# Kernel tuning notes

Hardware: AMD Instinct MI355X
Metric: run time of the kernel (lower is better)

## Reference

```python
import jax, jax.numpy as jnp
import numpy as np

NUM_STAB = 0.001  # numerical_stabilizer from relu_kernel_transformation


def relu_kernel(data, proj):
    """ReLU random-feature kernel: data [B,L,H,D], proj [M,D] -> [B,L,H,M]."""
    ratio = 1.0 / jnp.sqrt(jnp.asarray(proj.shape[0], jnp.float32))
    data_dash = ratio * jnp.einsum('blhd,md->blhm', data, proj)
    return jax.nn.relu(data_dash) + NUM_STAB


def setup_inputs() -> dict:
    key = jax.random.key(0)
    k1, k2, k3, k4 = jax.random.split(key, 4)
    B, L, H, D, M = 2, 4096, 8, 64, 256
    return {
        'query': jax.random.normal(k1, (B, L, H, D), jnp.float32),
        'key_t': jax.random.normal(k2, (B, L, H, D), jnp.float32),
        'value': jax.random.normal(k3, (B, L, H, D), jnp.float32),
        'projection_matrix': jax.random.normal(k4, (M, D), jnp.float32),
    }


def reference(query, key_t, value, projection_matrix):
    # Kernel feature maps [B,L,H,M]
    qp = relu_kernel(query, projection_matrix)
    kp = relu_kernel(key_t, projection_matrix)
    # Causal path operates in [L,B,H,*] layout
    qs = jnp.transpose(qp, (1, 0, 2, 3))     # [L,B,H,M]
    ks = jnp.transpose(kp, (1, 0, 2, 3))     # [L,B,H,M]
    vs = jnp.transpose(value, (1, 0, 2, 3))  # [L,B,H,D]

    B, H, M = qs.shape[1], qs.shape[2], qs.shape[3]
    D = vs.shape[3]
    init = (jnp.zeros((B, H, M, D), qs.dtype),  # running sum of k outer v
            jnp.zeros((B, H, M), qs.dtype))     # running sum of k

    def step(carry, inp):
        kv_sum, k_sum = carry
        q, k, v = inp  # [B,H,M], [B,H,M], [B,H,D]
        kv_sum = kv_sum + k[..., None] * v[..., None, :]
        k_sum = k_sum + k
        num = jnp.einsum('bhmd,bhm->bhd', kv_sum, q)  # causal numerator step
        den = jnp.einsum('bhm,bhm->bh', q, k_sum)     # causal denominator step
        return (kv_sum, k_sum), (num, den)

    _, (num, den) = jax.lax.scan(step, init, (qs, ks, vs))  # num [L,B,H,D], den [L,B,H]
    den = den[..., None]
    den = jnp.where(den <= 0.0, jnp.ones_like(den), den)
    out = num / den                      # [L,B,H,D]
    return jnp.transpose(out, (1, 0, 2, 3))  # [B,L,H,D]
```

## Files before the change

### kernel.cpp

```cpp
#include <hip/hip_runtime.h>
#include <hip/hip_bf16.h>


#define B_   2
#define L_   4096
#define H_   8
#define D_   64
#define M_   256
#define T_   128
#define C_   (L_ / T_)
#define NBH  (B_ * H_)
#define RATIO 0.0625f
#define STAB  0.001f
#define SVT  136
#define SQS  72

typedef __attribute__((ext_vector_type(8))) short short8;
typedef __attribute__((ext_vector_type(4))) float floatx4;

#define MFMA16(a, b, c) __builtin_amdgcn_mfma_f32_16x16x32_bf16(a, b, c, 0, 0, 0)

__device__ inline unsigned short f2bf(float x) {
    union { float f; unsigned u; } v; v.f = x;
    unsigned r = v.u + 0x7FFF + ((v.u >> 16) & 1);
    return (unsigned short)(r >> 16);
}
__device__ inline unsigned pack2bf(float a, float b) {
    __hip_bfloat162 h = __float22bfloat162_rn(make_float2(a, b));
    unsigned u; __builtin_memcpy(&u, &h, 4);
    return u;
}
__device__ inline short8 ldg8_bfs(const float* p) {
    float4 a = *(const float4*)p;
    float4 b = *(const float4*)(p + 4);
    short8 r;
    r[0] = (short)f2bf(a.x * RATIO); r[1] = (short)f2bf(a.y * RATIO);
    r[2] = (short)f2bf(a.z * RATIO); r[3] = (short)f2bf(a.w * RATIO);
    r[4] = (short)f2bf(b.x * RATIO); r[5] = (short)f2bf(b.y * RATIO);
    r[6] = (short)f2bf(b.z * RATIO); r[7] = (short)f2bf(b.w * RATIO);
    return r;
}
__device__ inline short8 ldg8_bf(const float* p) {
    float4 a = *(const float4*)p;
    float4 b = *(const float4*)(p + 4);
    short8 r;
    r[0] = (short)f2bf(a.x); r[1] = (short)f2bf(a.y);
    r[2] = (short)f2bf(a.z); r[3] = (short)f2bf(a.w);
    r[4] = (short)f2bf(b.x); r[5] = (short)f2bf(b.y);
    r[6] = (short)f2bf(b.z); r[7] = (short)f2bf(b.w);
    return r;
}

__global__ __launch_bounds__(512, 2)
void chunk_kernel(const float* __restrict__ key, const float* __restrict__ val,
                  const float* __restrict__ proj,
                  unsigned short* __restrict__ VTg, unsigned short* __restrict__ Pbf,
                  float* __restrict__ Ppart, float* __restrict__ Zpart) {
    const int c = blockIdx.x, bh = blockIdx.y;
    const int b = bh / H_, h = bh % H_;
    const int tid = threadIdx.x;
    const int w = tid >> 6, lane = tid & 63;
    const int l15 = lane & 15, quad = lane >> 4;

    __shared__ __align__(16) unsigned short SH[128 * SVT];
    __shared__ __align__(16) unsigned short KbfL[T_ * D_];
    unsigned short* VT  = SH;
    unsigned short* KpT = SH;

    const size_t rowstr = H_ * D_;
    const size_t base = ((size_t)b * L_ + (size_t)c * T_) * rowstr + (size_t)h * D_;

    for (int i = tid; i < T_ * 8; i += 512) {
        int t = i >> 3, d8 = (i & 7) * 8;
        short8 kv = ldg8_bfs(key + base + (size_t)t * rowstr + d8);
        int rt = t >> 4, l = t & 15, kk = d8 >> 5, q = (d8 & 31) >> 3;
        *(short8*)&KbfL[((rt * 2 + kk) * 64 + q * 16 + l) << 3] = kv;
    }
    for (int i = tid; i < T_ * 16; i += 512) {
        int t = i >> 4, d4 = (i & 15) * 4;
        float4 vv = *(const float4*)(val + base + (size_t)t * rowstr + d4);
        VT[(d4 + 0) * SVT + t] = f2bf(vv.x);
        VT[(d4 + 1) * SVT + t] = f2bf(vv.y);
        VT[(d4 + 2) * SVT + t] = f2bf(vv.z);
        VT[(d4 + 3) * SVT + t] = f2bf(vv.w);
    }
    __syncthreads();
    unsigned short* vout = VTg + ((size_t)bh * C_ + c) * (D_ * T_);
    for (int i = tid; i < D_ * 16; i += 512) {
        int d = i >> 4, tt = (i & 15) * 8;
        *(uint4*)(vout + d * T_ + tt) = *(const uint4*)&VT[d * SVT + tt];
    }
    const int dt_w = w >> 1;
    const int mt0 = (w & 1) * 4;
    short8 vf[4];
#pragma unroll
    for (int k4 = 0; k4 < 4; ++k4)
        vf[k4] = *(const short8*)&VT[(dt_w * 16 + l15) * SVT + k4 * 32 + quad * 8];
    if (c == 0 && tid < 256) {
        int i = bh * 256 + tid;
        float4 pv = *(const float4*)(proj + (size_t)i * 4);
        uint2 o; o.x = pack2bf(pv.x, pv.y); o.y = pack2bf(pv.z, pv.w);
        *(uint2*)(Pbf + (size_t)i * 4) = o;
    }
    __syncthreads();

    float* Pp = Ppart + ((size_t)bh * C_ + c) * (D_ * M_);

    for (int half = 0; half < 2; ++half) {
        const int mrow = half * 128 + w * 16 + l15;
        short8 pf0 = ldg8_bf(proj + (size_t)mrow * D_ + quad * 8);
        short8 pf1 = ldg8_bf(proj + (size_t)mrow * D_ + 32 + quad * 8);
        if (half) __syncthreads();
        float zp = 0.f;
#pragma unroll
        for (int rt = 0; rt < 8; ++rt) {
            short8 kf0 = *(const short8*)&KbfL[((rt * 2 + 0) * 64 + lane) << 3];
            short8 kf1 = *(const short8*)&KbfL[((rt * 2 + 1) * 64 + lane) << 3];
            floatx4 a = {0.f, 0.f, 0.f, 0.f};
            a = MFMA16(kf0, pf0, a);
            a = MFMA16(kf1, pf1, a);
            float k0 = fmaxf(a[0], 0.f) + STAB;
            float k1 = fmaxf(a[1], 0.f) + STAB;
            float k2 = fmaxf(a[2], 0.f) + STAB;
            float k3 = fmaxf(a[3], 0.f) + STAB;
            zp += (k0 + k1) + (k2 + k3);
            uint2 pk; pk.x = pack2bf(k0, k1); pk.y = pack2bf(k2, k3);
            *(uint2*)&KpT[(w * 16 + l15) * SVT + rt * 16 + quad * 4] = pk;
        }
        zp += __shfl_xor(zp, 16, 64);
        zp += __shfl_xor(zp, 32, 64);
        if (quad == 0)
            Zpart[((size_t)bh * C_ + c) * M_ + mrow] = zp;
        __syncthreads();

#pragma unroll
        for (int mt = 0; mt < 4; ++mt) {
            floatx4 acc = {0.f, 0.f, 0.f, 0.f};
#pragma unroll
            for (int k4 = 0; k4 < 4; ++k4) {
                short8 kb = *(const short8*)&KpT[((mt0 + mt) * 16 + l15) * SVT
                                                 + k4 * 32 + quad * 8];
                acc = MFMA16(vf[k4], kb, acc);
            }
            const int mcol = half * 128 + (mt0 + mt) * 16 + l15;
#pragma unroll
            for (int r = 0; r < 4; ++r)
                Pp[(size_t)(dt_w * 16 + quad * 4 + r) * M_ + mcol] = acc[r];
        }
    }
}

__global__ __launch_bounds__(256, 4)
void prefix_kernel(const float* __restrict__ Ppart, const float* __restrict__ Zpart,
                   unsigned short* __restrict__ S, float* __restrict__ Z) {
    const int g = blockIdx.x, bh = blockIdx.y;
    const int tid = threadIdx.x;
    if (g < 32) {
        const size_t dm = ((size_t)g * 256 + tid) * 2;
        const float* Pp = Ppart + (size_t)bh * C_ * (D_ * M_) + dm;
        unsigned short* Sp = S + (size_t)bh * C_ * (D_ * M_) + dm;
        float accx = 0.f, accy = 0.f;
#pragma unroll 8
        for (int c = 0; c < C_; ++c) {
            float2 p = *(const float2*)(Pp + (size_t)c * (D_ * M_));
            *(unsigned*)(Sp + (size_t)c * (D_ * M_)) = pack2bf(accx, accy);
            accx += p.x; accy += p.y;
        }
    } else {
        const float* Zp = Zpart + (size_t)bh * C_ * M_ + tid;
        float* Zo = Z + (size_t)bh * C_ * M_ + tid;
        float acc = 0.f;
#pragma unroll 8
        for (int c = 0; c < C_; ++c) {
            float z = Zp[(size_t)c * M_];
            Zo[(size_t)c * M_] = acc;
            acc += z;
        }
    }
}

__global__ __launch_bounds__(512, 2)
void phase3_kernel(const float* __restrict__ q, const float* __restrict__ key,
                   const unsigned short* __restrict__ VTg,
                   const unsigned short* __restrict__ Pbf,
                   const unsigned short* __restrict__ S, const float* __restrict__ Z,
                   float* __restrict__ out) {
    const int c = blockIdx.x, bh = blockIdx.y;
    const int b = bh / H_, h = bh % H_;
    const int tid = threadIdx.x;
    const int w = tid >> 6, lane = tid & 63;
    const int l15 = lane & 15, quad = lane >> 4;

    __shared__ __align__(16) unsigned short KpL[T_ * SVT];
    __shared__ __align__(16) unsigned short QpS[8 * 16 * SQS];

    const size_t rowstr = H_ * D_;
    const size_t base = ((size_t)b * L_ + (size_t)c * T_) * rowstr + (size_t)h * D_;
    const unsigned short* Sp = S + (size_t)(bh * C_ + c) * (M_ * D_);
    const float* Zp = Z + (size_t)(bh * C_ + c) * M_;
    const unsigned short* Vc = VTg + ((size_t)bh * C_ + c) * (D_ * T_);

    short8 qf[2], kf[2];
#pragma unroll
    for (int kk = 0; kk < 2; ++kk) {
        size_t ro = base + (size_t)(16 * w + l15) * rowstr + kk * 32 + quad * 8;
        qf[kk] = ldg8_bfs(q + ro);
        kf[kk] = ldg8_bfs(key + ro);
    }

    unsigned short* myQp = QpS + w * 16 * SQS;
    floatx4 num[4];
    floatx4 Aacc[8];
#pragma unroll
    for (int dt = 0; dt < 4; ++dt) { floatx4 z4 = {0.f,0.f,0.f,0.f}; num[dt] = z4; }
#pragma unroll
    for (int ct = 0; ct < 8; ++ct) { floatx4 z4 = {0.f,0.f,0.f,0.f}; Aacc[ct] = z4; }
    float dz[4] = {0.f, 0.f, 0.f, 0.f};

    for (int hh = 0; hh < 2; ++hh) {
        short8 qa[4];
#pragma unroll
        for (int fgl = 0; fgl < 2; ++fgl) {
            const int fg = 2 * hh + fgl;
#pragma unroll
            for (int ct = 0; ct < 4; ++ct) {
                const unsigned short* pp = Pbf + (size_t)(fg * 64 + ct * 16 + l15) * D_;
                short8 pf0 = *(const short8*)(pp + quad * 8);
                short8 pf1 = *(const short8*)(pp + 32 + quad * 8);
                floatx4 aq = {0.f, 0.f, 0.f, 0.f};
                aq = MFMA16(qf[0], pf0, aq);
                aq = MFMA16(qf[1], pf1, aq);
                floatx4 ak = {0.f, 0.f, 0.f, 0.f};
                ak = MFMA16(kf[0], pf0, ak);
                ak = MFMA16(kf[1], pf1, ak);
                const int mloc = fgl * 64 + ct * 16 + l15;
                float zv = Zp[hh * 128 + mloc];
#pragma unroll
                for (int r = 0; r < 4; ++r) {
                    float qpv = fmaxf(aq[r], 0.f) + STAB;
                    float kpv = fmaxf(ak[r], 0.f) + STAB;
                    myQp[(quad * 4 + r) * SQS + ct * 16 + l15] = f2bf(qpv);
                    KpL[(size_t)(16 * w + quad * 4 + r) * SVT + mloc] = f2bf(kpv);
                    dz[r] = fmaf(qpv, zv, dz[r]);
                }
            }
#pragma unroll
            for (int kk = 0; kk < 2; ++kk)
                qa[fgl * 2 + kk] = *(const short8*)&myQp[l15 * SQS + kk * 32 + quad * 8];
        }
#pragma unroll
        for (int dt = 0; dt < 4; ++dt)
#pragma unroll
            for (int kc = 0; kc < 4; ++kc) {
                short8 sb = *(const short8*)(Sp + (size_t)(dt * 16 + l15) * M_
                                             + hh * 128 + kc * 32 + quad * 8);
                num[dt] = MFMA16(qa[kc], sb, num[dt]);
            }
        __syncthreads();
#pragma unroll
        for (int ct = 0; ct < 8; ++ct) {
            if (ct <= w) {
#pragma unroll
                for (int kc = 0; kc < 4; ++kc) {
                    short8 kb = *(const short8*)&KpL[(size_t)(ct * 16 + l15) * SVT
                                                     + kc * 32 + quad * 8];
                    Aacc[ct] = MFMA16(qa[kc], kb, Aacc[ct]);
                }
            }
        }
        __syncthreads();
    }
#pragma unroll
    for (int r = 0; r < 4; ++r) {
        dz[r] += __shfl_xor(dz[r], 1, 64);
        dz[r] += __shfl_xor(dz[r], 2, 64);
        dz[r] += __shfl_xor(dz[r], 4, 64);
        dz[r] += __shfl_xor(dz[r], 8, 64);
    }

    unsigned short* AmL = KpL;
    float da[4] = {0.f, 0.f, 0.f, 0.f};
#pragma unroll
    for (int ct = 0; ct < 8; ++ct)
#pragma unroll
        for (int r = 0; r < 4; ++r) {
            float av = Aacc[ct][r];
            if (ct > w || (ct == w && l15 > quad * 4 + r)) av = 0.f;
            AmL[(size_t)(16 * w + quad * 4 + r) * SVT + ct * 16 + l15] = f2bf(av);
            da[r] += av;
        }
#pragma unroll
    for (int r = 0; r < 4; ++r) {
        da[r] += __shfl_xor(da[r], 1, 64);
        da[r] += __shfl_xor(da[r], 2, 64);
        da[r] += __shfl_xor(da[r], 4, 64);
        da[r] += __shfl_xor(da[r], 8, 64);
    }

    for (int k4 = 0; k4 <= (w >> 1); ++k4) {
        short8 am = *(const short8*)&AmL[(size_t)(16 * w + l15) * SVT
                                         + k4 * 32 + quad * 8];
#pragma unroll
        for (int dt = 0; dt < 4; ++dt) {
            short8 vb = *(const short8*)(Vc + (size_t)(dt * 16 + l15) * T_
                                         + k4 * 32 + quad * 8);
            num[dt] = MFMA16(am, vb, num[dt]);
        }
    }

#pragma unroll
    for (int r = 0; r < 4; ++r) {
        float den = da[r] + dz[r];
        if (den <= 0.f) den = 1.f;
        float inv = 1.f / den;
        int t = 16 * w + quad * 4 + r;
#pragma unroll
        for (int dt = 0; dt < 4; ++dt)
            out[base + (size_t)t * rowstr + dt * 16 + l15] = num[dt][r] * inv;
    }
}

extern "C" void kernel_launch(void* const* d_in, const int* in_sizes, int n_in,
                              void* d_out, int out_size, void* d_ws, size_t ws_size,
                              hipStream_t stream) {
    const float* q    = (const float*)d_in[0];
    const float* k    = (const float*)d_in[1];
    const float* v    = (const float*)d_in[2];
    const float* proj = (const float*)d_in[3];
    float* out = (float*)d_out;

    const size_t nS = (size_t)NBH * C_ * D_ * M_;
    const size_t nZ = (size_t)NBH * C_ * M_;
    const size_t nV = (size_t)NBH * C_ * D_ * T_;
    unsigned short* S     = (unsigned short*)d_ws;
    float*          Z     = (float*)(S + nS);
    unsigned short* VTg   = (unsigned short*)(Z + nZ);
    unsigned short* Pbf   = VTg + nV;
    float*          Ppart = (float*)(Pbf + (size_t)M_ * D_);
    float*          Zpart = Ppart + nS;

    chunk_kernel<<<dim3(C_, NBH), dim3(512), 0, stream>>>(k, v, proj, VTg, Pbf, Ppart, Zpart);
    prefix_kernel<<<dim3(33, NBH), dim3(256), 0, stream>>>(Ppart, Zpart, S, Z);
    phase3_kernel<<<dim3(C_, NBH), dim3(512), 0, stream>>>(q, k, VTg, Pbf, S, Z, out);
}
```

Baseline: 157.1 us.

## Fuse three phases into one cooperative persistent kernel with grid syncs

Merges the chunk, prefix-scan and output kernels into one cooperative kernel of 256 blocks, each handling two (chunk, bh) tiles, with grid-wide syncs between phases. The bf16 key tile is kept in shared memory across phases so the output phase does not reload and reconvert keys from global memory. This removes two kernel launches and their gaps. In exchange it runs at one block per CU, uses more LDS, and pays for two grid barriers.

```diff
diff --git a/kernel.cpp b/kernel.cpp
--- a/kernel.cpp
+++ b/kernel.cpp
@@ -1,5 +1,8 @@
 #include <hip/hip_runtime.h>
 #include <hip/hip_bf16.h>
+#include <hip/hip_cooperative_groups.h>
+
+namespace cg = cooperative_groups;
 
 
 #define B_   2
@@ -51,272 +54,279 @@
     return r;
 }
 
-__global__ __launch_bounds__(512, 2)
-void chunk_kernel(const float* __restrict__ key, const float* __restrict__ val,
-                  const float* __restrict__ proj,
+__global__ __launch_bounds__(512, 1)
+void fused_kernel(const float* __restrict__ q, const float* __restrict__ key,
+                  const float* __restrict__ val, const float* __restrict__ proj,
                   unsigned short* __restrict__ VTg, unsigned short* __restrict__ Pbf,
-                  float* __restrict__ Ppart, float* __restrict__ Zpart) {
-    const int c = blockIdx.x, bh = blockIdx.y;
-    const int b = bh / H_, h = bh % H_;
+                  float* __restrict__ Ppart, float* __restrict__ Zpart,
+                  unsigned short* __restrict__ S, float* __restrict__ Z,
+                  float* __restrict__ out) {
+    cg::grid_group grid = cg::this_grid();
+    const int fid = blockIdx.x;
     const int tid = threadIdx.x;
     const int w = tid >> 6, lane = tid & 63;
     const int l15 = lane & 15, quad = lane >> 4;
 
+    __shared__ __align__(16) unsigned short Kbf2[2][T_ * D_];
     __shared__ __align__(16) unsigned short SH[128 * SVT];
-    __shared__ __align__(16) unsigned short KbfL[T_ * D_];
-    unsigned short* VT  = SH;
-    unsigned short* KpT = SH;
+    __shared__ __align__(16) unsigned short QpS[8 * 16 * SQS];
 
     const size_t rowstr = H_ * D_;
-    const size_t base = ((size_t)b * L_ + (size_t)c * T_) * rowstr + (size_t)h * D_;
-
-    for (int i = tid; i < T_ * 8; i += 512) {
-        int t = i >> 3, d8 = (i & 7) * 8;
-        short8 kv = ldg8_bfs(key + base + (size_t)t * rowstr + d8);
-        int rt = t >> 4, l = t & 15, kk = d8 >> 5, q = (d8 & 31) >> 3;
-        *(short8*)&KbfL[((rt * 2 + kk) * 64 + q * 16 + l) << 3] = kv;
+
+    for (int pi = 0; pi < 2; ++pi) {
+        if (pi) __syncthreads();
+        const int p = fid + pi * 256;
+        const int c = p & 31, bh = p >> 5;
+        const int b = bh / H_, h = bh % H_;
+        const size_t base = ((size_t)b * L_ + (size_t)c * T_) * rowstr + (size_t)h * D_;
+        unsigned short* VT  = SH;
+        unsigned short* KpT = SH;
+        unsigned short* KbfL = Kbf2[pi];
+
+        for (int i = tid; i < T_ * 8; i += 512) {
+            int t = i >> 3, d8 = (i & 7) * 8;
+            short8 kv = ldg8_bfs(key + base + (size_t)t * rowstr + d8);
+            int rt = t >> 4, l = t & 15, kk = d8 >> 5, qq = (d8 & 31) >> 3;
+            *(short8*)&KbfL[((rt * 2 + kk) * 64 + qq * 16 + l) << 3] = kv;
+        }
+        for (int i = tid; i < T_ * 16; i += 512) {
+            int t = i >> 4, d4 = (i & 15) * 4;
+            float4 vv = *(const float4*)(val + base + (size_t)t * rowstr + d4);
+            VT[(d4 + 0) * SVT + t] = f2bf(vv.x);
+            VT[(d4 + 1) * SVT + t] = f2bf(vv.y);
+            VT[(d4 + 2) * SVT + t] = f2bf(vv.z);
+            VT[(d4 + 3) * SVT + t] = f2bf(vv.w);
+        }
+        __syncthreads();
+        unsigned short* vout = VTg + ((size_t)bh * C_ + c) * (D_ * T_);
+        for (int i = tid; i < D_ * 16; i += 512) {
+            int d = i >> 4, tt = (i & 15) * 8;
+            *(uint4*)(vout + d * T_ + tt) = *(const uint4*)&VT[d * SVT + tt];
+        }
+        const int dt_w = w >> 1;
+        const int mt0 = (w & 1) * 4;
+        short8 vf[4];
+#pragma unroll
+        for (int k4 = 0; k4 < 4; ++k4)
+            vf[k4] = *(const short8*)&VT[(dt_w * 16 + l15) * SVT + k4 * 32 + quad * 8];
+        if (c == 0 && tid < 256) {
+            int i = bh * 256 + tid;
+            float4 pv = *(const float4*)(proj + (size_t)i * 4);
+            uint2 o; o.x = pack2bf(pv.x, pv.y); o.y = pack2bf(pv.z, pv.w);
+            *(uint2*)(Pbf + (size_t)i * 4) = o;
+        }
+        __syncthreads();
+
+        float* Pp = Ppart + ((size_t)bh * C_ + c) * (D_ * M_);
+
+        for (int half = 0; half < 2; ++half) {
+            const int mrow = half * 128 + w * 16 + l15;
+            short8 pf0 = ldg8_bf(proj + (size_t)mrow * D_ + quad * 8);
+            short8 pf1 = ldg8_bf(proj + (size_t)mrow * D_ + 32 + quad * 8);
+            if (half) __syncthreads();
+            float zp = 0.f;
+#pragma unroll
+            for (int rt = 0; rt < 8; ++rt) {
+                short8 kf0 = *(const short8*)&KbfL[((rt * 2 + 0) * 64 + lane) << 3];
+                short8 kf1 = *(const short8*)&KbfL[((rt * 2 + 1) * 64 + lane) << 3];
+                floatx4 a = {0.f, 0.f, 0.f, 0.f};
+                a = MFMA16(kf0, pf0, a);
+                a = MFMA16(kf1, pf1, a);
+                float k0 = fmaxf(a[0], 0.f) + STAB;
+                float k1 = fmaxf(a[1], 0.f) + STAB;
+                float k2 = fmaxf(a[2], 0.f) + STAB;
+                float k3 = fmaxf(a[3], 0.f) + STAB;
+                zp += (k0 + k1) + (k2 + k3);
+                uint2 pk; pk.x = pack2bf(k0, k1); pk.y = pack2bf(k2, k3);
+                *(uint2*)&KpT[(w * 16 + l15) * SVT + rt * 16 + quad * 4] = pk;
+            }
+            zp += __shfl_xor(zp, 16, 64);
+            zp += __shfl_xor(zp, 32, 64);
+            if (quad == 0)
+                Zpart[((size_t)bh * C_ + c) * M_ + mrow] = zp;
+            __syncthreads();
+
+#pragma unroll
+            for (int mt = 0; mt < 4; ++mt) {
+                floatx4 acc = {0.f, 0.f, 0.f, 0.f};
+#pragma unroll
+                for (int k4 = 0; k4 < 4; ++k4) {
+                    short8 kb = *(const short8*)&KpT[((mt0 + mt) * 16 + l15) * SVT
+                                                     + k4 * 32 + quad * 8];
+                    acc = MFMA16(vf[k4], kb, acc);
+                }
+                const int mcol = half * 128 + (mt0 + mt) * 16 + l15;
+#pragma unroll
+                for (int r = 0; r < 4; ++r)
+                    Pp[(size_t)(dt_w * 16 + quad * 4 + r) * M_ + mcol] = acc[r];
+            }
+        }
     }
-    for (int i = tid; i < T_ * 16; i += 512) {
-        int t = i >> 4, d4 = (i & 15) * 4;
-        float4 vv = *(const float4*)(val + base + (size_t)t * rowstr + d4);
-        VT[(d4 + 0) * SVT + t] = f2bf(vv.x);
-        VT[(d4 + 1) * SVT + t] = f2bf(vv.y);
-        VT[(d4 + 2) * SVT + t] = f2bf(vv.z);
-        VT[(d4 + 3) * SVT + t] = f2bf(vv.w);
+    __threadfence();
+    grid.sync();
+
+    {
+        const size_t DM = (size_t)D_ * M_;
+        for (int it = 0; it < 2; ++it) {
+            size_t col = ((size_t)(it * 256 + fid)) * 512 + tid;
+            int bh = (int)(col >> 14);
+            size_t dm = col & (DM - 1);
+            const float* Pp = Ppart + (size_t)bh * C_ * DM + dm;
+            unsigned short* Sp = S + (size_t)bh * C_ * DM + dm;
+            float acc = 0.f;
+#pragma unroll 8
+            for (int cc = 0; cc < C_; ++cc) {
+                float pv = Pp[(size_t)cc * DM];
+                Sp[(size_t)cc * DM] = f2bf(acc);
+                acc += pv;
+            }
+        }
+        if (fid < 8) {
+            int zcol = fid * 512 + tid;
+            int bh = zcol >> 8, m = zcol & 255;
+            const float* Zp = Zpart + (size_t)bh * C_ * M_ + m;
+            float* Zo = Z + (size_t)bh * C_ * M_ + m;
+            float acc = 0.f;
+#pragma unroll 8
+            for (int cc = 0; cc < C_; ++cc) {
+                float zv = Zp[(size_t)cc * M_];
+                Zo[(size_t)cc * M_] = acc;
+                acc += zv;
+            }
+        }
     }
-    __syncthreads();
-    unsigned short* vout = VTg + ((size_t)bh * C_ + c) * (D_ * T_);
-    for (int i = tid; i < D_ * 16; i += 512) {
-        int d = i >> 4, tt = (i & 15) * 8;
-        *(uint4*)(vout + d * T_ + tt) = *(const uint4*)&VT[d * SVT + tt];
-    }
-    const int dt_w = w >> 1;
-    const int mt0 = (w & 1) * 4;
-    short8 vf[4];
-#pragma unroll
-    for (int k4 = 0; k4 < 4; ++k4)
-        vf[k4] = *(const short8*)&VT[(dt_w * 16 + l15) * SVT + k4 * 32 + quad * 8];
-    if (c == 0 && tid < 256) {
-        int i = bh * 256 + tid;
-        float4 pv = *(const float4*)(proj + (size_t)i * 4);
-        uint2 o; o.x = pack2bf(pv.x, pv.y); o.y = pack2bf(pv.z, pv.w);
-        *(uint2*)(Pbf + (size_t)i * 4) = o;
-    }
-    __syncthreads();
-
-    float* Pp = Ppart + ((size_t)bh * C_ + c) * (D_ * M_);
-
-    for (int half = 0; half < 2; ++half) {
-        const int mrow = half * 128 + w * 16 + l15;
-        short8 pf0 = ldg8_bf(proj + (size_t)mrow * D_ + quad * 8);
-        short8 pf1 = ldg8_bf(proj + (size_t)mrow * D_ + 32 + quad * 8);
-        if (half) __syncthreads();
-        float zp = 0.f;
-#pragma unroll
-        for (int rt = 0; rt < 8; ++rt) {
-            short8 kf0 = *(const short8*)&KbfL[((rt * 2 + 0) * 64 + lane) << 3];
-            short8 kf1 = *(const short8*)&KbfL[((rt * 2 + 1) * 64 + lane) << 3];
-            floatx4 a = {0.f, 0.f, 0.f, 0.f};
-            a = MFMA16(kf0, pf0, a);
-            a = MFMA16(kf1, pf1, a);
-            float k0 = fmaxf(a[0], 0.f) + STAB;
-            float k1 = fmaxf(a[1], 0.f) + STAB;
-            float k2 = fmaxf(a[2], 0.f) + STAB;
-            float k3 = fmaxf(a[3], 0.f) + STAB;
-            zp += (k0 + k1) + (k2 + k3);
-            uint2 pk; pk.x = pack2bf(k0, k1); pk.y = pack2bf(k2, k3);
-            *(uint2*)&KpT[(w * 16 + l15) * SVT + rt * 16 + quad * 4] = pk;
-        }
-        zp += __shfl_xor(zp, 16, 64);
-        zp += __shfl_xor(zp, 32, 64);
-        if (quad == 0)
-            Zpart[((size_t)bh * C_ + c) * M_ + mrow] = zp;
-        __syncthreads();
-
-#pragma unroll
-        for (int mt = 0; mt < 4; ++mt) {
-            floatx4 acc = {0.f, 0.f, 0.f, 0.f};
-#pragma unroll
-            for (int k4 = 0; k4 < 4; ++k4) {
-                short8 kb = *(const short8*)&KpT[((mt0 + mt) * 16 + l15) * SVT
-                                                 + k4 * 32 + quad * 8];
-                acc = MFMA16(vf[k4], kb, acc);
-            }
-            const int mcol = half * 128 + (mt0 + mt) * 16 + l15;
-#pragma unroll
-            for (int r = 0; r < 4; ++r)
-                Pp[(size_t)(dt_w * 16 + quad * 4 + r) * M_ + mcol] = acc[r];
-        }
-    }
-}
-
-__global__ __launch_bounds__(256, 4)
-void prefix_kernel(const float* __restrict__ Ppart, const float* __restrict__ Zpart,
-                   unsigned short* __restrict__ S, float* __restrict__ Z) {
-    const int g = blockIdx.x, bh = blockIdx.y;
-    const int tid = threadIdx.x;
-    if (g < 32) {
-        const size_t dm = ((size_t)g * 256 + tid) * 2;
-        const float* Pp = Ppart + (size_t)bh * C_ * (D_ * M_) + dm;
-        unsigned short* Sp = S + (size_t)bh * C_ * (D_ * M_) + dm;
-        float accx = 0.f, accy = 0.f;
-#pragma unroll 8
-        for (int c = 0; c < C_; ++c) {
-            float2 p = *(const float2*)(Pp + (size_t)c * (D_ * M_));
-            *(unsigned*)(Sp + (size_t)c * (D_ * M_)) = pack2bf(accx, accy);
-            accx += p.x; accy += p.y;
-        }
-    } else {
-        const float* Zp = Zpart + (size_t)bh * C_ * M_ + tid;
-        float* Zo = Z + (size_t)bh * C_ * M_ + tid;
-        float acc = 0.f;
-#pragma unroll 8
-        for (int c = 0; c < C_; ++c) {
-            float z = Zp[(size_t)c * M_];
-            Zo[(size_t)c * M_] = acc;
-            acc += z;
-        }
-    }
-}
-
-__global__ __launch_bounds__(512, 2)
-void phase3_kernel(const float* __restrict__ q, const float* __restrict__ key,
-                   const unsigned short* __restrict__ VTg,
-                   const unsigned short* __restrict__ Pbf,
-                   const unsigned short* __restrict__ S, const float* __restrict__ Z,
-                   float* __restrict__ out) {
-    const int c = blockIdx.x, bh = blockIdx.y;
-    const int b = bh / H_, h = bh % H_;
-    const int tid = threadIdx.x;
-    const int w = tid >> 6, lane = tid & 63;
-    const int l15 = lane & 15, quad = lane >> 4;
-
-    __shared__ __align__(16) unsigned short KpL[T_ * SVT];
-    __shared__ __align__(16) unsigned short QpS[8 * 16 * SQS];
-
-    const size_t rowstr = H_ * D_;
-    const size_t base = ((size_t)b * L_ + (size_t)c * T_) * rowstr + (size_t)h * D_;
-    const unsigned short* Sp = S + (size_t)(bh * C_ + c) * (M_ * D_);
-    const float* Zp = Z + (size_t)(bh * C_ + c) * M_;
-    const unsigned short* Vc = VTg + ((size_t)bh * C_ + c) * (D_ * T_);
-
-    short8 qf[2], kf[2];
-#pragma unroll
-    for (int kk = 0; kk < 2; ++kk) {
-        size_t ro = base + (size_t)(16 * w + l15) * rowstr + kk * 32 + quad * 8;
-        qf[kk] = ldg8_bfs(q + ro);
-        kf[kk] = ldg8_bfs(key + ro);
-    }
-
-    unsigned short* myQp = QpS + w * 16 * SQS;
-    floatx4 num[4];
-    floatx4 Aacc[8];
-#pragma unroll
-    for (int dt = 0; dt < 4; ++dt) { floatx4 z4 = {0.f,0.f,0.f,0.f}; num[dt] = z4; }
-#pragma unroll
-    for (int ct = 0; ct < 8; ++ct) { floatx4 z4 = {0.f,0.f,0.f,0.f}; Aacc[ct] = z4; }
-    float dz[4] = {0.f, 0.f, 0.f, 0.f};
-
-    for (int hh = 0; hh < 2; ++hh) {
-        short8 qa[4];
-#pragma unroll
-        for (int fgl = 0; fgl < 2; ++fgl) {
-            const int fg = 2 * hh + fgl;
-#pragma unroll
-            for (int ct = 0; ct < 4; ++ct) {
-                const unsigned short* pp = Pbf + (size_t)(fg * 64 + ct * 16 + l15) * D_;
-                short8 pf0 = *(const short8*)(pp + quad * 8);
-                short8 pf1 = *(const short8*)(pp + 32 + quad * 8);
-                floatx4 aq = {0.f, 0.f, 0.f, 0.f};
-                aq = MFMA16(qf[0], pf0, aq);
-                aq = MFMA16(qf[1], pf1, aq);
-                floatx4 ak = {0.f, 0.f, 0.f, 0.f};
-                ak = MFMA16(kf[0], pf0, ak);
-                ak = MFMA16(kf[1], pf1, ak);
-                const int mloc = fgl * 64 + ct * 16 + l15;
-                float zv = Zp[hh * 128 + mloc];
-#pragma unroll
-                for (int r = 0; r < 4; ++r) {
-                    float qpv = fmaxf(aq[r], 0.f) + STAB;
-                    float kpv = fmaxf(ak[r], 0.f) + STAB;
-                    myQp[(quad * 4 + r) * SQS + ct * 16 + l15] = f2bf(qpv);
-                    KpL[(size_t)(16 * w + quad * 4 + r) * SVT + mloc] = f2bf(kpv);
-                    dz[r] = fmaf(qpv, zv, dz[r]);
+    __threadfence();
+    grid.sync();
+
+    for (int pi = 0; pi < 2; ++pi) {
+        if (pi) __syncthreads();
+        const int p = fid + pi * 256;
+        const int c = p & 31, bh = p >> 5;
+        const int b = bh / H_, h = bh % H_;
+        const size_t base = ((size_t)b * L_ + (size_t)c * T_) * rowstr + (size_t)h * D_;
+        const unsigned short* Sp = S + (size_t)(bh * C_ + c) * (M_ * D_);
+        const float* Zp = Z + (size_t)(bh * C_ + c) * M_;
+        const unsigned short* Vc = VTg + ((size_t)bh * C_ + c) * (D_ * T_);
+        unsigned short* KpL = SH;
+        const unsigned short* KbfL = Kbf2[pi];
+
+        short8 qf[2], kf[2];
+#pragma unroll
+        for (int kk = 0; kk < 2; ++kk) {
+            qf[kk] = ldg8_bfs(q + base + (size_t)(16 * w + l15) * rowstr + kk * 32 + quad * 8);
+            kf[kk] = *(const short8*)&KbfL[((w * 2 + kk) * 64 + lane) << 3];
+        }
+
+        unsigned short* myQp = QpS + w * 16 * SQS;
+        floatx4 num[4];
+        floatx4 Aacc[8];
+#pragma unroll
+        for (int dt = 0; dt < 4; ++dt) { floatx4 z4 = {0.f,0.f,0.f,0.f}; num[dt] = z4; }
+#pragma unroll
+        for (int ct = 0; ct < 8; ++ct) { floatx4 z4 = {0.f,0.f,0.f,0.f}; Aacc[ct] = z4; }
+        float dz[4] = {0.f, 0.f, 0.f, 0.f};
+
+        for (int hh = 0; hh < 2; ++hh) {
+            short8 qa[4];
+#pragma unroll
+            for (int fgl = 0; fgl < 2; ++fgl) {
+                const int fg = 2 * hh + fgl;
+#pragma unroll
+                for (int ct = 0; ct < 4; ++ct) {
+                    const unsigned short* pp = Pbf + (size_t)(fg * 64 + ct * 16 + l15) * D_;
+                    short8 pf0 = *(const short8*)(pp + quad * 8);
+                    short8 pf1 = *(const short8*)(pp + 32 + quad * 8);
+                    floatx4 aq = {0.f, 0.f, 0.f, 0.f};
+                    aq = MFMA16(qf[0], pf0, aq);
+                    aq = MFMA16(qf[1], pf1, aq);
+                    floatx4 ak = {0.f, 0.f, 0.f, 0.f};
+                    ak = MFMA16(kf[0], pf0, ak);
+                    ak = MFMA16(kf[1], pf1, ak);
+                    const int mloc = fgl * 64 + ct * 16 + l15;
+                    float zv = Zp[hh * 128 + mloc];
+#pragma unroll
+                    for (int r = 0; r < 4; ++r) {
+                        float qpv = fmaxf(aq[r], 0.f) + STAB;
+                        float kpv = fmaxf(ak[r], 0.f) + STAB;
+                        myQp[(quad * 4 + r) * SQS + ct * 16 + l15] = f2bf(qpv);
+                        KpL[(size_t)(16 * w + quad * 4 + r) * SVT + mloc] = f2bf(kpv);
+                        dz[r] = fmaf(qpv, zv, dz[r]);
+                    }
                 }
-            }
-#pragma unroll
-            for (int kk = 0; kk < 2; ++kk)
-                qa[fgl * 2 + kk] = *(const short8*)&myQp[l15 * SQS + kk * 32 + quad * 8];
-        }
-#pragma unroll
-        for (int dt = 0; dt < 4; ++dt)
-#pragma unroll
-            for (int kc = 0; kc < 4; ++kc) {
-                short8 sb = *(const short8*)(Sp + (size_t)(dt * 16 + l15) * M_
-                                             + hh * 128 + kc * 32 + quad * 8);
-                num[dt] = MFMA16(qa[kc], sb, num[dt]);
-            }
-        __syncthreads();
-#pragma unroll
-        for (int ct = 0; ct < 8; ++ct) {
-            if (ct <= w) {
+#pragma unroll
+                for (int kk = 0; kk < 2; ++kk)
+                    qa[fgl * 2 + kk] = *(const short8*)&myQp[l15 * SQS + kk * 32 + quad * 8];
+            }
+#pragma unroll
+            for (int dt = 0; dt < 4; ++dt)
 #pragma unroll
                 for (int kc = 0; kc < 4; ++kc) {
-                    short8 kb = *(const short8*)&KpL[(size_t)(ct * 16 + l15) * SVT
-                                                     + kc * 32 + quad * 8];
-                    Aacc[ct] = MFMA16(qa[kc], kb, Aacc[ct]);
+                    short8 sb = *(const short8*)(Sp + (size_t)(dt * 16 + l15) * M_
+                                                 + hh * 128 + kc * 32 + quad * 8);
+                    num[dt] = MFMA16(qa[kc], sb, num[dt]);
                 }
-            }
-        }
-        __syncthreads();
-    }
-#pragma unroll
-    for (int r = 0; r < 4; ++r) {
-        dz[r] += __shfl_xor(dz[r], 1, 64);
-        dz[r] += __shfl_xor(dz[r], 2, 64);
-        dz[r] += __shfl_xor(dz[r], 4, 64);
-        dz[r] += __shfl_xor(dz[r], 8, 64);
-    }
-
-    unsigned short* AmL = KpL;
-    float da[4] = {0.f, 0.f, 0.f, 0.f};
-#pragma unroll
-    for (int ct = 0; ct < 8; ++ct)
+            __syncthreads();
+#pragma unroll
+            for (int ct = 0; ct < 8; ++ct) {
+                if (ct <= w) {
+#pragma unroll
+                    for (int kc = 0; kc < 4; ++kc) {
+                        short8 kb = *(const short8*)&KpL[(size_t)(ct * 16 + l15) * SVT
+                                                         + kc * 32 + quad * 8];
+                        Aacc[ct] = MFMA16(qa[kc], kb, Aacc[ct]);
+                    }
+                }
+            }
+            __syncthreads();
+        }
 #pragma unroll
         for (int r = 0; r < 4; ++r) {
-            float av = Aacc[ct][r];
-            if (ct > w || (ct == w && l15 > quad * 4 + r)) av = 0.f;
-            AmL[(size_t)(16 * w + quad * 4 + r) * SVT + ct * 16 + l15] = f2bf(av);
-            da[r] += av;
-        }
-#pragma unroll
-    for (int r = 0; r < 4; ++r) {
-        da[r] += __shfl_xor(da[r], 1, 64);
-        da[r] += __shfl_xor(da[r], 2, 64);
-        da[r] += __shfl_xor(da[r], 4, 64);
-        da[r] += __shfl_xor(da[r], 8, 64);
-    }
-
-    for (int k4 = 0; k4 <= (w >> 1); ++k4) {
-        short8 am = *(const short8*)&AmL[(size_t)(16 * w + l15) * SVT
-                                         + k4 * 32 + quad * 8];
-#pragma unroll
-        for (int dt = 0; dt < 4; ++dt) {
-            short8 vb = *(const short8*)(Vc + (size_t)(dt * 16 + l15) * T_
-                                         + k4 * 32 + quad * 8);
-            num[dt] = MFMA16(am, vb, num[dt]);
-        }
-    }
-
-#pragma unroll
-    for (int r = 0; r < 4; ++r) {
-        float den = da[r] + dz[r];
-        if (den <= 0.f) den = 1.f;
-        float inv = 1.f / den;
-        int t = 16 * w + quad * 4 + r;
-#pragma unroll
-        for (int dt = 0; dt < 4; ++dt)
-            out[base + (size_t)t * rowstr + dt * 16 + l15] = num[dt][r] * inv;
+            dz[r] += __shfl_xor(dz[r], 1, 64);
+            dz[r] += __shfl_xor(dz[r], 2, 64);
+            dz[r] += __shfl_xor(dz[r], 4, 64);
+            dz[r] += __shfl_xor(dz[r], 8, 64);
+        }
+
+        unsigned short* AmL = KpL;
+        float da[4] = {0.f, 0.f, 0.f, 0.f};
+#pragma unroll
+        for (int ct = 0; ct < 8; ++ct)
+#pragma unroll
+            for (int r = 0; r < 4; ++r) {
+                float av = Aacc[ct][r];
+                if (ct > w || (ct == w && l15 > quad * 4 + r)) av = 0.f;
+                AmL[(size_t)(16 * w + quad * 4 + r) * SVT + ct * 16 + l15] = f2bf(av);
+                da[r] += av;
+            }
+#pragma unroll
+        for (int r = 0; r < 4; ++r) {
+            da[r] += __shfl_xor(da[r], 1, 64);
+            da[r] += __shfl_xor(da[r], 2, 64);
+            da[r] += __shfl_xor(da[r], 4, 64);
+            da[r] += __shfl_xor(da[r], 8, 64);
+        }
+
+        for (int k4 = 0; k4 <= (w >> 1); ++k4) {
+            short8 am = *(const short8*)&AmL[(size_t)(16 * w + l15) * SVT
+                                             + k4 * 32 + quad * 8];
+#pragma unroll
+            for (int dt = 0; dt < 4; ++dt) {
+                short8 vb = *(const short8*)(Vc + (size_t)(dt * 16 + l15) * T_
+                                             + k4 * 32 + quad * 8);
+                num[dt] = MFMA16(am, vb, num[dt]);
+            }
+        }
+
+#pragma unroll
+        for (int r = 0; r < 4; ++r) {
+            float den = da[r] + dz[r];
+            if (den <= 0.f) den = 1.f;
+            float inv = 1.f / den;
+            int t = 16 * w + quad * 4 + r;
+#pragma unroll
+            for (int dt = 0; dt < 4; ++dt)
+                out[base + (size_t)t * rowstr + dt * 16 + l15] = num[dt][r] * inv;
+        }
     }
 }
 
@@ -339,7 +349,9 @@
     float*          Ppart = (float*)(Pbf + (size_t)M_ * D_);
     float*          Zpart = Ppart + nS;
 
-    chunk_kernel<<<dim3(C_, NBH), dim3(512), 0, stream>>>(k, v, proj, VTg, Pbf, Ppart, Zpart);
-    prefix_kernel<<<dim3(33, NBH), dim3(256), 0, stream>>>(Ppart, Zpart, S, Z);
-    phase3_kernel<<<dim3(C_, NBH), dim3(512), 0, stream>>>(q, k, VTg, Pbf, S, Z, out);
-}
+    void* args[] = {(void*)&q, (void*)&k, (void*)&v, (void*)&proj,
+                    (void*)&VTg, (void*)&Pbf, (void*)&Ppart, (void*)&Zpart,
+                    (void*)&S, (void*)&Z, (void*)&out};
+    hipLaunchCooperativeKernel((void*)fused_kernel, dim3(256), dim3(512),
+                               args, 0, stream);
+}
```

Measured after the change: 343.3 us. +118.5%, slower.
